# Kernel optimization log

Measured on AMD Instinct MI355X. Metric: run time of the kernel, lower is better.

## Reference

```python
import jax, jax.numpy as jnp
import numpy as np

B = 8192
D = 1024
NUM_HEADS = 16
HEAD_DIM = D // NUM_HEADS  # 64; only used as the softmax scale


def setup_inputs() -> dict:
    key = jax.random.key(0)
    ks = jax.random.split(key, 7)
    s = 1.0 / np.sqrt(D)
    return {
        "x": jax.random.normal(ks[0], (B, D), dtype=jnp.float32),
        "Wq": jax.random.normal(ks[1], (D, D), dtype=jnp.float32) * s,
        "bq": jax.random.normal(ks[2], (D,), dtype=jnp.float32) * s,
        "Wk": jax.random.normal(ks[3], (D, D), dtype=jnp.float32) * s,
        "bk": jax.random.normal(ks[4], (D,), dtype=jnp.float32) * s,
        "Wv": jax.random.normal(ks[5], (D, D), dtype=jnp.float32) * s,
        "bv": jax.random.normal(ks[6], (D,), dtype=jnp.float32) * s,
    }


def reference(x, Wq, bq, Wk, bk, Wv, bv):
    # Faithful to the torch module: x is 2D [B, D]; attention is over the batch axis.
    # nn.Linear computes x @ W.T + b
    Q = x @ Wq.T + bq            # [B, D]
    K = x @ Wk.T + bk            # [B, D]
    V = x @ Wv.T + bv            # [B, D]
    scale = 1.0 / jnp.sqrt(jnp.float32(HEAD_DIM))
    energy = (Q @ K.T) * scale   # [B, B]
    attn = jax.nn.softmax(energy, axis=-1)
    out = attn @ V               # [B, D]
    # torch: x.permute(0,1).contiguous().view(B, seq_len, -1) -> [B, D, 1]
    return out.reshape(B, D, 1)
```

## Files before the change

kernel.cpp:

```cpp
#include <hip/hip_runtime.h>
#include <hip/hip_bf16.h>

typedef _Float16 half_t;
typedef _Float16 f16x8 __attribute__((ext_vector_type(8)));
typedef _Float16 f16x4 __attribute__((ext_vector_type(4)));
typedef float f32x4 __attribute__((ext_vector_type(4)));

#define B_ROWS 8192
#define D_DIM  1024

__device__ __forceinline__ void gload_lds16(const void* g, void* l)
{
    __builtin_amdgcn_global_load_lds((const __attribute__((address_space(1))) void*)g,
                                     (__attribute__((address_space(3))) void*)l, 16, 0, 0);
}

__global__ __launch_bounds__(256)
void cvt_f32_f16(const float* __restrict__ in, half_t* __restrict__ out, int n)
{
    int i = (blockIdx.x * 256 + threadIdx.x) * 4;
    int stride = gridDim.x * 256 * 4;
    for (; i < n; i += stride) {
        float4 v = *(const float4*)&in[i];
        f16x4 o;
        o[0] = (half_t)v.x; o[1] = (half_t)v.y; o[2] = (half_t)v.z; o[3] = (half_t)v.w;
        *(f16x4*)&out[i] = o;
    }
}

__global__ __launch_bounds__(256)
void transpose_h(const half_t* __restrict__ in, half_t* __restrict__ out, int R, int C)
{
    __shared__ half_t t[64][65];
    int tilesC = C >> 6;
    int bc = blockIdx.x % tilesC;
    int br = blockIdx.x / tilesC;
    int r0 = br * 64, c0 = bc * 64;
    for (int e = threadIdx.x; e < 64 * 64; e += 256) {
        int r = e >> 6, c = e & 63;
        t[r][c] = in[(size_t)(r0 + r) * C + (c0 + c)];
    }
    __syncthreads();
    for (int e = threadIdx.x; e < 64 * 64; e += 256) {
        int r = e >> 6, c = e & 63;
        out[(size_t)(c0 + r) * R + (r0 + c)] = t[c][r];
    }
}

template<int EPI>
__device__ __forceinline__ void gemm8_core(
    const half_t* __restrict__ A, const half_t* __restrict__ Bm,
    const float* __restrict__ bias, void* __restrict__ Out,
    int lda, int ldb, int ldc, float scale,
    int row0, int col0, int ktile0, int nkt)
{
    __shared__ __align__(16) half_t As[4 * 8192];
    __shared__ __align__(16) half_t Bs[4 * 8192];

    const int tid  = threadIdx.x;
    const int lane = tid & 63;
    const int wid  = tid >> 6;
    const int wr   = wid >> 2;
    const int wcn  = wid & 3;
    const int l15  = lane & 15;
    const int l4   = lane >> 4;

    const int trow  = tid >> 3;
    const int tslot = (tid & 7) ^ (trow & 7);
    const char* Apan[2] = { (const char*)(A + (size_t)row0 * lda),
                            (const char*)(A + (size_t)(row0 + 128) * lda) };
    const char* Bpan[2] = { (const char*)(Bm + (size_t)col0 * ldb),
                            (const char*)(Bm + (size_t)(col0 + 128) * ldb) };
    const size_t aoff[2] = { (size_t)trow * lda * 2 + (size_t)tslot * 16,
                             (size_t)(trow + 64) * lda * 2 + (size_t)tslot * 16 };
    const size_t boff[2] = { (size_t)trow * ldb * 2 + (size_t)tslot * 16,
                             (size_t)(trow + 64) * ldb * 2 + (size_t)tslot * 16 };
    const int dstb[2] = { tid * 16, 8192 + tid * 16 };

    auto stageA = [&](int h, int s, int buf) {
        char* d = (char*)(As + (buf * 2 + h) * 8192);
        const char* g = Apan[h] + (size_t)(ktile0 + s) * 128;
        gload_lds16(g + aoff[0], d + dstb[0]);
        gload_lds16(g + aoff[1], d + dstb[1]);
    };
    auto stageB = [&](int h, int s, int buf) {
        char* d = (char*)(Bs + (buf * 2 + h) * 8192);
        const char* g = Bpan[h] + (size_t)(ktile0 + s) * 128;
        gload_lds16(g + boff[0], d + dstb[0]);
        gload_lds16(g + boff[1], d + dstb[1]);
    };
    auto rdA = [&](int mm, int kb, const half_t* base) -> f16x8 {
        int rih  = mm * 32 + wr * 16 + l15;
        int byte = rih * 128 + (((kb * 4 + l4) ^ (rih & 7)) << 4);
        return *(const f16x8*)((const char*)base + byte);
    };
    auto rdB = [&](int nn, int kb, const half_t* base) -> f16x8 {
        int rih  = nn * 64 + wcn * 16 + l15;
        int byte = rih * 128 + (((kb * 4 + l4) ^ (rih & 7)) << 4);
        return *(const f16x8*)((const char*)base + byte);
    };

    f32x4 acc[8][4] = {};
    f16x8 af[4][2], bf[2][2];

    {
        int s1 = (nkt > 1) ? 1 : 0;
        stageA(0, 0, 0); stageB(0, 0, 0); stageA(1, 0, 0); stageB(1, 0, 0);
        stageA(0, s1, 1); stageB(0, s1, 1);
    }
    asm volatile("s_waitcnt vmcnt(4)" ::: "memory");
    asm volatile("s_barrier" ::: "memory");

    for (int t = 0; t < nkt; ++t) {
        const int buf = t & 1;
        const half_t* A0 = As + (buf * 2 + 0) * 8192;
        const half_t* A1 = As + (buf * 2 + 1) * 8192;
        const half_t* B0 = Bs + (buf * 2 + 0) * 8192;
        const half_t* B1 = Bs + (buf * 2 + 1) * 8192;
        int t1  = t + 1; int t1s = (t1 < nkt) ? t1 : nkt - 1; int b1 = t1 & 1;
        int t2  = t + 2; int t2s = (t2 < nkt) ? t2 : nkt - 1;

        #pragma unroll
        for (int m = 0; m < 4; ++m) { af[m][0] = rdA(m, 0, A0); af[m][1] = rdA(m, 1, A0); }
        #pragma unroll
        for (int n = 0; n < 2; ++n) { bf[n][0] = rdB(n, 0, B0); bf[n][1] = rdB(n, 1, B0); }
        stageA(1, t1s, b1);
        asm volatile("s_barrier" ::: "memory");
        __builtin_amdgcn_s_setprio(1);
        #pragma unroll
        for (int kb = 0; kb < 2; ++kb)
            #pragma unroll
            for (int m = 0; m < 4; ++m)
                #pragma unroll
                for (int n = 0; n < 2; ++n)
                    acc[m][n] = __builtin_amdgcn_mfma_f32_16x16x32_f16(af[m][kb], bf[n][kb], acc[m][n], 0, 0, 0);
        __builtin_amdgcn_s_setprio(0);
        asm volatile("s_barrier" ::: "memory");

        #pragma unroll
        for (int n = 0; n < 2; ++n) { bf[n][0] = rdB(n, 0, B1); bf[n][1] = rdB(n, 1, B1); }
        stageB(1, t1s, b1);
        asm volatile("s_barrier" ::: "memory");
        __builtin_amdgcn_s_setprio(1);
        #pragma unroll
        for (int kb = 0; kb < 2; ++kb)
            #pragma unroll
            for (int m = 0; m < 4; ++m)
                #pragma unroll
                for (int n = 0; n < 2; ++n)
                    acc[m][n + 2] = __builtin_amdgcn_mfma_f32_16x16x32_f16(af[m][kb], bf[n][kb], acc[m][n + 2], 0, 0, 0);
        __builtin_amdgcn_s_setprio(0);
        asm volatile("s_barrier" ::: "memory");

        #pragma unroll
        for (int m = 0; m < 4; ++m) { af[m][0] = rdA(m, 0, A1); af[m][1] = rdA(m, 1, A1); }
        #pragma unroll
        for (int n = 0; n < 2; ++n) { bf[n][0] = rdB(n, 0, B0); bf[n][1] = rdB(n, 1, B0); }
        stageA(0, t2s, buf);
        asm volatile("s_barrier" ::: "memory");
        __builtin_amdgcn_s_setprio(1);
        #pragma unroll
        for (int kb = 0; kb < 2; ++kb)
            #pragma unroll
            for (int m = 0; m < 4; ++m)
                #pragma unroll
                for (int n = 0; n < 2; ++n)
                    acc[m + 4][n] = __builtin_amdgcn_mfma_f32_16x16x32_f16(af[m][kb], bf[n][kb], acc[m + 4][n], 0, 0, 0);
        __builtin_amdgcn_s_setprio(0);
        asm volatile("s_barrier" ::: "memory");

        #pragma unroll
        for (int n = 0; n < 2; ++n) { bf[n][0] = rdB(n, 0, B1); bf[n][1] = rdB(n, 1, B1); }
        stageB(0, t2s, buf);
        asm volatile("s_barrier" ::: "memory");
        __builtin_amdgcn_s_setprio(1);
        #pragma unroll
        for (int kb = 0; kb < 2; ++kb)
            #pragma unroll
            for (int m = 0; m < 4; ++m)
                #pragma unroll
                for (int n = 0; n < 2; ++n)
                    acc[m + 4][n + 2] = __builtin_amdgcn_mfma_f32_16x16x32_f16(af[m][kb], bf[n][kb], acc[m + 4][n + 2], 0, 0, 0);
        __builtin_amdgcn_s_setprio(0);
        asm volatile("s_waitcnt vmcnt(4)" ::: "memory");
        asm volatile("s_barrier" ::: "memory");
    }

    #pragma unroll
    for (int m = 0; m < 8; ++m) {
        int grow_base = row0 + m * 32 + wr * 16 + l4 * 4;
        #pragma unroll
        for (int n = 0; n < 4; ++n) {
            int gcol = col0 + n * 64 + wcn * 16 + l15;
            float badd = (EPI == 0) ? bias[gcol] : 0.0f;
            #pragma unroll
            for (int r = 0; r < 4; ++r) {
                float v = acc[m][n][r] * scale + badd;
                size_t idx = (size_t)(grow_base + r) * ldc + gcol;
                if (EPI == 2) ((float*)Out)[idx] = v;
                else          ((half_t*)Out)[idx] = (half_t)v;
            }
        }
    }
}

template<int EPI>
__global__ __launch_bounds__(512, 2)
void gemm8(const half_t* __restrict__ A, const half_t* __restrict__ Bm,
           const float* __restrict__ bias, void* __restrict__ Out,
           int lda, int ldb, int ldc, float scale, int nkt)
{
    int nwg = gridDim.x * gridDim.y;
    int bid = blockIdx.y * gridDim.x + blockIdx.x;
    if ((nwg & 7) == 0) { int c = nwg >> 3; bid = (bid & 7) * c + (bid >> 3); }
    int bx = bid % gridDim.x, by = bid / gridDim.x;
    gemm8_core<EPI>(A, Bm, bias, Out, lda, ldb, ldc, scale, by * 256, bx * 256, 0, nkt);
}

__global__ __launch_bounds__(512, 2)
void gemm8_qkv(const half_t* __restrict__ xh,
               const half_t* __restrict__ Wq, const half_t* __restrict__ Wk, const half_t* __restrict__ Wv,
               const float* __restrict__ bq, const float* __restrict__ bk, const float* __restrict__ bv,
               half_t* __restrict__ Q, half_t* __restrict__ K, half_t* __restrict__ V)
{
    int z = blockIdx.z;
    const half_t* W = (z == 0) ? Wq : (z == 1) ? Wk : Wv;
    const float*  b = (z == 0) ? bq : (z == 1) ? bk : bv;
    half_t*       O = (z == 0) ? Q  : (z == 1) ? K  : V;
    gemm8_core<0>(xh, W, b, O, D_DIM, D_DIM, D_DIM, 1.0f,
                  blockIdx.y * 256, blockIdx.x * 256, 0, D_DIM / 64);
}

__global__ __launch_bounds__(512, 2)
void gemm8_pv(const half_t* __restrict__ S, const half_t* __restrict__ Vt,
              float* __restrict__ part0, float* __restrict__ part1)
{
    int z = blockIdx.z;
    float* O = z ? part1 : part0;
    gemm8_core<2>(S, Vt, nullptr, O, B_ROWS, B_ROWS, D_DIM, 1.0f,
                  blockIdx.y * 256, blockIdx.x * 256, z * (B_ROWS / 128), B_ROWS / 128);
}

__global__ __launch_bounds__(256)
void add_f32(const float* __restrict__ a, float* __restrict__ out, int n)
{
    int i = (blockIdx.x * 256 + threadIdx.x) * 4;
    int stride = gridDim.x * 256 * 4;
    for (; i < n; i += stride) {
        float4 x = *(const float4*)&out[i];
        float4 y = *(const float4*)&a[i];
        x.x += y.x; x.y += y.y; x.z += y.z; x.w += y.w;
        *(float4*)&out[i] = x;
    }
}

__global__ __launch_bounds__(256)
void softmax_rows(half_t* __restrict__ S, int ncol)
{
    const int row = blockIdx.x;
    half_t* srow = S + (size_t)row * ncol;
    const int tid = threadIdx.x;

    float ev[32];
    float m = -1e30f;
    #pragma unroll
    for (int it = 0; it < 4; ++it) {
        int j = it * 2048 + tid * 8;
        f16x8 v = *(const f16x8*)&srow[j];
        #pragma unroll
        for (int t = 0; t < 8; ++t) {
            float f = (float)v[t];
            ev[it * 8 + t] = f;
            m = fmaxf(m, f);
        }
    }
    #pragma unroll
    for (int o = 32; o; o >>= 1) m = fmaxf(m, __shfl_down(m, o));
    __shared__ float redm[8];
    __shared__ float reds[8];
    if ((tid & 63) == 0) redm[tid >> 6] = m;
    __syncthreads();
    m = fmaxf(fmaxf(redm[0], redm[1]), fmaxf(redm[2], redm[3]));

    float s = 0.0f;
    #pragma unroll
    for (int e = 0; e < 32; ++e) {
        float ex = __expf(ev[e] - m);
        ev[e] = ex;
        s += ex;
    }
    #pragma unroll
    for (int o = 32; o; o >>= 1) s += __shfl_down(s, o);
    if ((tid & 63) == 0) reds[tid >> 6] = s;
    __syncthreads();
    s = reds[0] + reds[1] + reds[2] + reds[3];
    float inv = 1.0f / s;

    #pragma unroll
    for (int it = 0; it < 4; ++it) {
        int j = it * 2048 + tid * 8;
        f16x8 o8;
        #pragma unroll
        for (int t = 0; t < 8; ++t) o8[t] = (half_t)(ev[it * 8 + t] * inv);
        *(f16x8*)&srow[j] = o8;
    }
}

extern "C" void kernel_launch(void* const* d_in, const int* in_sizes, int n_in,
                              void* d_out, int out_size, void* d_ws, size_t ws_size,
                              hipStream_t stream)
{
    const float* x  = (const float*)d_in[0];
    const float* Wq = (const float*)d_in[1];
    const float* bq = (const float*)d_in[2];
    const float* Wk = (const float*)d_in[3];
    const float* bk = (const float*)d_in[4];
    const float* Wv = (const float*)d_in[5];
    const float* bv = (const float*)d_in[6];
    float* out = (float*)d_out;

    const int Bb = B_ROWS, Dd = D_DIM;

    char* w = (char*)d_ws;
    size_t off = 0;
    auto carve = [&](size_t bytes) {
        void* p = w + off;
        off += (bytes + 255) & ~(size_t)255;
        return p;
    };
    half_t* xh  = (half_t*)carve((size_t)Bb * Dd * 2);
    half_t* Wqh = (half_t*)carve((size_t)Dd * Dd * 2);
    half_t* Wkh = (half_t*)carve((size_t)Dd * Dd * 2);
    half_t* Wvh = (half_t*)carve((size_t)Dd * Dd * 2);
    half_t* Qh  = (half_t*)carve((size_t)Bb * Dd * 2);
    half_t* Kh  = (half_t*)carve((size_t)Bb * Dd * 2);
    half_t* Vh  = (half_t*)carve((size_t)Bb * Dd * 2);
    half_t* S   = (half_t*)carve((size_t)Bb * Bb * 2);
    half_t* Vt  = xh;
    float*  part1 = (float*)Qh;

    cvt_f32_f16<<<2048, 256, 0, stream>>>(x,  xh,  Bb * Dd);
    cvt_f32_f16<<<1024, 256, 0, stream>>>(Wq, Wqh, Dd * Dd);
    cvt_f32_f16<<<1024, 256, 0, stream>>>(Wk, Wkh, Dd * Dd);
    cvt_f32_f16<<<1024, 256, 0, stream>>>(Wv, Wvh, Dd * Dd);

    dim3 gqkv(Dd / 256, Bb / 256, 3);
    gemm8_qkv<<<gqkv, 512, 0, stream>>>(xh, Wqh, Wkh, Wvh, bq, bk, bv, Qh, Kh, Vh);

    transpose_h<<<(Dd / 64) * (Bb / 64), 256, 0, stream>>>(Vh, Vt, Bb, Dd);

    dim3 gs(Bb / 256, Bb / 256);
    gemm8<1><<<gs, 512, 0, stream>>>(Qh, Kh, nullptr, S, Dd, Dd, Bb, 0.125f, Dd / 64);

    softmax_rows<<<Bb, 256, 0, stream>>>(S, Bb);

    dim3 gpv(Dd / 256, Bb / 256, 2);
    gemm8_pv<<<gpv, 512, 0, stream>>>(S, Vt, out, part1);
    add_f32<<<2048, 256, 0, stream>>>(part1, out, Bb * Dd);
}
```

Measured before the change: 445.5 us.

## Software-pipeline LDS fragment reads one quadrant ahead of MFMA compute

Result: slower. 474.3 us (+6.5%).

```diff
diff --git a/kernel.cpp b/kernel.cpp
--- a/kernel.cpp
+++ b/kernel.cpp
@@ -71,10 +71,8 @@
                             (const char*)(A + (size_t)(row0 + 128) * lda) };
     const char* Bpan[2] = { (const char*)(Bm + (size_t)col0 * ldb),
                             (const char*)(Bm + (size_t)(col0 + 128) * ldb) };
-    const size_t aoff[2] = { (size_t)trow * lda * 2 + (size_t)tslot * 16,
-                             (size_t)(trow + 64) * lda * 2 + (size_t)tslot * 16 };
-    const size_t boff[2] = { (size_t)trow * ldb * 2 + (size_t)tslot * 16,
-                             (size_t)(trow + 64) * ldb * 2 + (size_t)tslot * 16 };
+    const int aoff[2] = { trow * lda * 2 + tslot * 16, (trow + 64) * lda * 2 + tslot * 16 };
+    const int boff[2] = { trow * ldb * 2 + tslot * 16, (trow + 64) * ldb * 2 + tslot * 16 };
     const int dstb[2] = { tid * 16, 8192 + tid * 16 };
 
     auto stageA = [&](int h, int s, int buf) {
@@ -101,31 +99,42 @@
     };
 
     f32x4 acc[8][4] = {};
-    f16x8 af[4][2], bf[2][2];
+    f16x8 afA[4][2];
+    f16x8 afN[4][2];
+    f16x8 bfP[2][2];
+    f16x8 bfQ[2][2];
 
     {
         int s1 = (nkt > 1) ? 1 : 0;
         stageA(0, 0, 0); stageB(0, 0, 0); stageA(1, 0, 0); stageB(1, 0, 0);
         stageA(0, s1, 1); stageB(0, s1, 1);
     }
-    asm volatile("s_waitcnt vmcnt(4)" ::: "memory");
+    asm volatile("s_waitcnt vmcnt(8)" ::: "memory");
     asm volatile("s_barrier" ::: "memory");
+    {
+        const half_t* A0 = As;
+        const half_t* B0 = Bs;
+        #pragma unroll
+        for (int m = 0; m < 4; ++m) { afA[m][0] = rdA(m, 0, A0); afA[m][1] = rdA(m, 1, A0); }
+        #pragma unroll
+        for (int n = 0; n < 2; ++n) { bfP[n][0] = rdB(n, 0, B0); bfP[n][1] = rdB(n, 1, B0); }
+    }
 
     for (int t = 0; t < nkt; ++t) {
         const int buf = t & 1;
-        const half_t* A0 = As + (buf * 2 + 0) * 8192;
-        const half_t* A1 = As + (buf * 2 + 1) * 8192;
-        const half_t* B0 = Bs + (buf * 2 + 0) * 8192;
-        const half_t* B1 = Bs + (buf * 2 + 1) * 8192;
-        int t1  = t + 1; int t1s = (t1 < nkt) ? t1 : nkt - 1; int b1 = t1 & 1;
-        int t2  = t + 2; int t2s = (t2 < nkt) ? t2 : nkt - 1;
-
-        #pragma unroll
-        for (int m = 0; m < 4; ++m) { af[m][0] = rdA(m, 0, A0); af[m][1] = rdA(m, 1, A0); }
-        #pragma unroll
-        for (int n = 0; n < 2; ++n) { bf[n][0] = rdB(n, 0, B0); bf[n][1] = rdB(n, 1, B0); }
+        const int b1  = buf ^ 1;
+        const half_t* A1c = As + (buf * 2 + 1) * 8192;
+        const half_t* B1c = Bs + (buf * 2 + 1) * 8192;
+        const half_t* A0n = As + (b1 * 2 + 0) * 8192;
+        const half_t* B0n = Bs + (b1 * 2 + 0) * 8192;
+        int t1s = (t + 1 < nkt) ? t + 1 : nkt - 1;
+        int t2s = (t + 2 < nkt) ? t + 2 : nkt - 1;
+
+        asm volatile("s_waitcnt vmcnt(4)" ::: "memory");
+        asm volatile("s_barrier" ::: "memory");
         stageA(1, t1s, b1);
-        asm volatile("s_barrier" ::: "memory");
+        #pragma unroll
+        for (int n = 0; n < 2; ++n) { bfQ[n][0] = rdB(n, 0, B1c); bfQ[n][1] = rdB(n, 1, B1c); }
         __builtin_amdgcn_s_setprio(1);
         #pragma unroll
         for (int kb = 0; kb < 2; ++kb)
@@ -133,14 +142,13 @@
             for (int m = 0; m < 4; ++m)
                 #pragma unroll
                 for (int n = 0; n < 2; ++n)
-                    acc[m][n] = __builtin_amdgcn_mfma_f32_16x16x32_f16(af[m][kb], bf[n][kb], acc[m][n], 0, 0, 0);
+                    acc[m][n] = __builtin_amdgcn_mfma_f32_16x16x32_f16(afA[m][kb], bfP[n][kb], acc[m][n], 0, 0, 0);
         __builtin_amdgcn_s_setprio(0);
+
         asm volatile("s_barrier" ::: "memory");
-
-        #pragma unroll
-        for (int n = 0; n < 2; ++n) { bf[n][0] = rdB(n, 0, B1); bf[n][1] = rdB(n, 1, B1); }
         stageB(1, t1s, b1);
-        asm volatile("s_barrier" ::: "memory");
+        #pragma unroll
+        for (int m = 0; m < 4; ++m) { afN[m][0] = rdA(m, 0, A1c); afN[m][1] = rdA(m, 1, A1c); }
         __builtin_amdgcn_s_setprio(1);
         #pragma unroll
         for (int kb = 0; kb < 2; ++kb)
@@ -148,16 +156,14 @@
             for (int m = 0; m < 4; ++m)
                 #pragma unroll
                 for (int n = 0; n < 2; ++n)
-                    acc[m][n + 2] = __builtin_amdgcn_mfma_f32_16x16x32_f16(af[m][kb], bf[n][kb], acc[m][n + 2], 0, 0, 0);
+                    acc[m][n + 2] = __builtin_amdgcn_mfma_f32_16x16x32_f16(afA[m][kb], bfQ[n][kb], acc[m][n + 2], 0, 0, 0);
         __builtin_amdgcn_s_setprio(0);
+
+        asm volatile("s_waitcnt vmcnt(4)" ::: "memory");
         asm volatile("s_barrier" ::: "memory");
-
-        #pragma unroll
-        for (int m = 0; m < 4; ++m) { af[m][0] = rdA(m, 0, A1); af[m][1] = rdA(m, 1, A1); }
-        #pragma unroll
-        for (int n = 0; n < 2; ++n) { bf[n][0] = rdB(n, 0, B0); bf[n][1] = rdB(n, 1, B0); }
         stageA(0, t2s, buf);
-        asm volatile("s_barrier" ::: "memory");
+        #pragma unroll
+        for (int m = 0; m < 4; ++m) { afA[m][0] = rdA(m, 0, A0n); afA[m][1] = rdA(m, 1, A0n); }
         __builtin_amdgcn_s_setprio(1);
         #pragma unroll
         for (int kb = 0; kb < 2; ++kb)
@@ -165,14 +171,13 @@
             for (int m = 0; m < 4; ++m)
                 #pragma unroll
                 for (int n = 0; n < 2; ++n)
-                    acc[m + 4][n] = __builtin_amdgcn_mfma_f32_16x16x32_f16(af[m][kb], bf[n][kb], acc[m + 4][n], 0, 0, 0);
+                    acc[m + 4][n] = __builtin_amdgcn_mfma_f32_16x16x32_f16(afN[m][kb], bfP[n][kb], acc[m + 4][n], 0, 0, 0);
         __builtin_amdgcn_s_setprio(0);
+
         asm volatile("s_barrier" ::: "memory");
-
-        #pragma unroll
-        for (int n = 0; n < 2; ++n) { bf[n][0] = rdB(n, 0, B1); bf[n][1] = rdB(n, 1, B1); }
         stageB(0, t2s, buf);
-        asm volatile("s_barrier" ::: "memory");
+        #pragma unroll
+        for (int n = 0; n < 2; ++n) { bfP[n][0] = rdB(n, 0, B0n); bfP[n][1] = rdB(n, 1, B0n); }
         __builtin_amdgcn_s_setprio(1);
         #pragma unroll
         for (int kb = 0; kb < 2; ++kb)
@@ -180,10 +185,8 @@
             for (int m = 0; m < 4; ++m)
                 #pragma unroll
                 for (int n = 0; n < 2; ++n)
-                    acc[m + 4][n + 2] = __builtin_amdgcn_mfma_f32_16x16x32_f16(af[m][kb], bf[n][kb], acc[m + 4][n + 2], 0, 0, 0);
+                    acc[m + 4][n + 2] = __builtin_amdgcn_mfma_f32_16x16x32_f16(afN[m][kb], bfQ[n][kb], acc[m + 4][n + 2], 0, 0, 0);
         __builtin_amdgcn_s_setprio(0);
-        asm volatile("s_waitcnt vmcnt(4)" ::: "memory");
-        asm volatile("s_barrier" ::: "memory");
     }
 
     #pragma unroll
```
